# Performance work log

Measured on AMD Instinct MI355X. Metric: run time of the kernel, lower is better.

Reference implementation:

```python
import jax, jax.numpy as jnp
import numpy as np

N_NODES = 50000
N_EDGES = 1600000
DIM = 128
BN_EPS = 1e-5


def setup_inputs() -> dict:
    key = jax.random.key(0)
    k1, k2, k3 = jax.random.split(key, 3)
    x = jax.random.normal(k1, (N_NODES, DIM), dtype=jnp.float32)
    edge_index = jax.random.randint(k2, (2, N_EDGES), 0, N_NODES, dtype=jnp.int32)
    W = jax.random.normal(k3, (DIM, DIM), dtype=jnp.float32) / np.float32(np.sqrt(DIM))
    b = jnp.zeros((DIM,), dtype=jnp.float32)
    gamma = jnp.ones((DIM,), dtype=jnp.float32)
    beta = jnp.zeros((DIM,), dtype=jnp.float32)
    return {"x": x, "W": W, "b": b, "gamma": gamma, "beta": beta, "edge_index": edge_index}


def reference(x, W, b, gamma, beta, edge_index):
    """ResGCNBlock: relu(BN(GCNConv(x, edge_index))) + x (PyG GCNConv semantics)."""
    n = x.shape[0]
    # GCNConv: linear transform first
    h = x @ W  # [N, D]
    # add self-loops
    loop = jnp.arange(n, dtype=edge_index.dtype)
    src = jnp.concatenate([edge_index[0], loop])  # [E+N]
    dst = jnp.concatenate([edge_index[1], loop])
    # symmetric normalization: deg over targets (edge weight = 1)
    deg = jax.ops.segment_sum(jnp.ones_like(dst, dtype=h.dtype), dst, num_segments=n)
    dinv = jax.lax.rsqrt(jnp.maximum(deg, 1e-12))  # deg >= 1 due to self-loops
    norm = dinv[src] * dinv[dst]  # [E+N]
    # gather -> scale -> scatter-add
    agg = jax.ops.segment_sum(h[src] * norm[:, None], dst, num_segments=n) + b  # [N, D]
    # BatchNorm1d (training mode: batch stats over node dim, biased variance)
    mean = jnp.mean(agg, axis=0)
    var = jnp.mean(jnp.square(agg - mean), axis=0)
    y = gamma * (agg - mean) * jax.lax.rsqrt(var + BN_EPS) + beta
    return jax.nn.relu(y) + x
```

## Files before the change

kernel.cpp:

```cpp
#include <hip/hip_runtime.h>

#define DIM 128

__device__ __forceinline__ float bf_to_f(unsigned short v) {
    return __uint_as_float(((unsigned int)v) << 16);
}
__device__ __forceinline__ unsigned short f_to_bf(float f) {
    unsigned int u = __float_as_uint(f);
    u += 0x7FFFu + ((u >> 16) & 1u);
    return (unsigned short)(u >> 16);
}
__device__ __forceinline__ bool probe_bf16(const void* gamma) {
    return *reinterpret_cast<const unsigned int*>(gamma) != 0x3F800000u;
}

__global__ __launch_bounds__(256) void k_deg(const int* __restrict__ ei,
                                             int* __restrict__ deg, int E) {
    int t = blockIdx.x * 256 + threadIdx.x;
    if (t < E) atomicAdd(&deg[ei[E + t]], 1);
}
__global__ __launch_bounds__(256) void k_dinv(const int* __restrict__ deg,
                                              float* __restrict__ dinv, int N) {
    int t = blockIdx.x * 256 + threadIdx.x;
    if (t < N) dinv[t] = rsqrtf((float)deg[t] + 1.0f);
}

#define EPB 4096

__global__ __launch_bounds__(256) void k_cbhist(const int* __restrict__ ei,
                                                int* __restrict__ thist, int E) {
    __shared__ int hist[256];
    const int t = threadIdx.x;
    const int e0 = blockIdx.x * EPB;
    hist[t] = 0;
    __syncthreads();
    #pragma unroll
    for (int u = 0; u < 16; u++) {
        const int i = e0 + t + u * 256;
        if (i < E) atomicAdd(&hist[((unsigned int)ei[E + i]) >> 8], 1);
    }
    __syncthreads();
    if (hist[t] > 0) atomicAdd(&thist[t], hist[t]);
}

__global__ __launch_bounds__(256) void k_bscan2(const int* __restrict__ thist,
                                                int* __restrict__ bbase,
                                                int* __restrict__ ccur) {
    __shared__ int sh[256];
    const int t = threadIdx.x;
    const int v = thist[t];
    sh[t] = v;
    __syncthreads();
    for (int off = 1; off < 256; off <<= 1) {
        int u = (t >= off) ? sh[t - off] : 0;
        __syncthreads();
        sh[t] += u;
        __syncthreads();
    }
    bbase[t + 1] = sh[t];
    ccur[t] = sh[t] - v;
    if (t == 0) bbase[0] = 0;
}

__global__ __launch_bounds__(256) void k_partition(
    const int* __restrict__ ei, int* __restrict__ ccur,
    unsigned int* __restrict__ epart, int E)
{
    __shared__ int hist[256];
    __shared__ int scan_tmp[256];
    __shared__ int lbase[256];
    __shared__ int lcur[256];
    __shared__ int gbase[256];
    __shared__ unsigned int sorted[EPB];
    const int t = threadIdx.x;
    const int e0 = blockIdx.x * EPB;
    const int ecount = min(EPB, E - e0);
    hist[t] = 0; lcur[t] = 0;
    __syncthreads();

    unsigned int ent[16];
    #pragma unroll
    for (int u = 0; u < 16; u++) {
        const int i = e0 + t + u * 256;
        if (i < E) {
            const unsigned int src = (unsigned int)ei[i];
            const unsigned int dst = (unsigned int)ei[E + i];
            const unsigned int cb = dst >> 8;
            ent[u] = src | ((dst & 255u) << 16) | (cb << 24);
            atomicAdd(&hist[cb], 1);
        } else ent[u] = 0xFFFFFFFFu;
    }
    __syncthreads();
    scan_tmp[t] = hist[t];
    __syncthreads();
    for (int off = 1; off < 256; off <<= 1) {
        int v = (t >= off) ? scan_tmp[t - off] : 0;
        __syncthreads();
        scan_tmp[t] += v;
        __syncthreads();
    }
    lbase[t] = scan_tmp[t] - hist[t];
    __syncthreads();
    #pragma unroll
    for (int u = 0; u < 16; u++) {
        if (ent[u] != 0xFFFFFFFFu) {
            const int cb = (int)(ent[u] >> 24);
            const int pos = lbase[cb] + atomicAdd(&lcur[cb], 1);
            sorted[pos] = ent[u];
        }
    }
    if (hist[t] > 0) gbase[t] = atomicAdd(&ccur[t], hist[t]);
    __syncthreads();
    for (int s = t; s < ecount; s += 256) {
        const unsigned int e = sorted[s];
        const int cb = (int)(e >> 24);
        epart[gbase[cb] + (s - lbase[cb])] = e;
    }
}

__global__ __launch_bounds__(256) void k_fine2(
    const unsigned int* __restrict__ epart, const int* __restrict__ bbase,
    int* __restrict__ rowptr, float* __restrict__ dinv,
    int* __restrict__ esrc, int N)
{
    __shared__ int ldeg[256];
    __shared__ int sh[256];
    __shared__ int lex[256];
    __shared__ int lcur[256];
    const int cb = blockIdx.x;
    const int t = threadIdx.x;
    const int beg = bbase[cb];
    const int end = bbase[cb + 1];
    ldeg[t] = 0; lcur[t] = 0;
    __syncthreads();

    for (int i = beg + t; i < end; i += 256)
        atomicAdd(&ldeg[(epart[i] >> 16) & 255u], 1);
    __syncthreads();
    sh[t] = ldeg[t];
    __syncthreads();
    for (int off = 1; off < 256; off <<= 1) {
        int v = (t >= off) ? sh[t - off] : 0;
        __syncthreads();
        sh[t] += v;
        __syncthreads();
    }
    lex[t] = sh[t] - ldeg[t];
    __syncthreads();

    const int node = (cb << 8) + t;
    if (node < N) {
        rowptr[node] = beg + lex[t];
        dinv[node] = rsqrtf((float)ldeg[t] + 1.0f);
        if (node == N - 1) rowptr[N] = beg + lex[t] + ldeg[t];
    }

    for (int i = beg + t; i < end; i += 256) {
        const unsigned int e = epart[i];
        const int d = (int)((e >> 16) & 255u);
        const int pos = beg + lex[d] + atomicAdd(&lcur[d], 1);
        esrc[pos] = (int)(e & 0xFFFFu);
    }
}

__global__ __launch_bounds__(256, 4) void k_gemm(
    const void* __restrict__ xv, const void* __restrict__ Wv,
    const void* __restrict__ bv, const void* __restrict__ probe,
    const float* __restrict__ dinv, unsigned short* __restrict__ h,
    float* __restrict__ agg, int N)
{
    const bool isbf = probe_bf16(probe);
    __shared__ __align__(16) unsigned short Wsb[DIM * 64];
    __shared__ __align__(16) float xs[64 * 132];
    const int t  = threadIdx.x;
    const int ch = blockIdx.x & 1;
    const int r0 = (blockIdx.x >> 1) * 64;

    if (isbf) {
        const unsigned short* W = (const unsigned short*)Wv;
        for (int s = 4 * t; s < DIM * 64; s += 1024) {
            const int k = s >> 6, c = s & 63;
            *reinterpret_cast<ushort4*>(Wsb + s) =
                *reinterpret_cast<const ushort4*>(W + k * DIM + ch * 64 + c);
        }
    } else {
        const float* W = (const float*)Wv;
        for (int s = 4 * t; s < DIM * 64; s += 1024) {
            const int k = s >> 6, c = s & 63;
            const float4 w = *reinterpret_cast<const float4*>(W + k * DIM + ch * 64 + c);
            ushort4 p;
            p.x = f_to_bf(w.x); p.y = f_to_bf(w.y);
            p.z = f_to_bf(w.z); p.w = f_to_bf(w.w);
            *reinterpret_cast<ushort4*>(Wsb + s) = p;
        }
    }
    for (int idx = 4 * t; idx < 64 * DIM; idx += 1024) {
        const int row = idx >> 7, k = idx & 127;
        const int r = r0 + row;
        float4 v = make_float4(0.f, 0.f, 0.f, 0.f);
        if (r < N) {
            if (isbf) {
                ushort4 u = *reinterpret_cast<const ushort4*>(
                    (const unsigned short*)xv + (size_t)r * DIM + k);
                v.x = bf_to_f(u.x); v.y = bf_to_f(u.y);
                v.z = bf_to_f(u.z); v.w = bf_to_f(u.w);
            } else {
                v = *reinterpret_cast<const float4*>((const float*)xv + (size_t)r * DIM + k);
            }
        }
        *reinterpret_cast<float4*>(xs + row * 132 + k) = v;
    }
    __syncthreads();

    const int c4 = t & 15;
    const int rg = t >> 4;
    float acc[4][4] = {{0,0,0,0},{0,0,0,0},{0,0,0,0},{0,0,0,0}};
    #pragma unroll 2
    for (int k = 0; k < DIM; k += 4) {
        const ushort4 wu0 = *reinterpret_cast<const ushort4*>(Wsb + (k + 0) * 64 + 4 * c4);
        const ushort4 wu1 = *reinterpret_cast<const ushort4*>(Wsb + (k + 1) * 64 + 4 * c4);
        const ushort4 wu2 = *reinterpret_cast<const ushort4*>(Wsb + (k + 2) * 64 + 4 * c4);
        const ushort4 wu3 = *reinterpret_cast<const ushort4*>(Wsb + (k + 3) * 64 + 4 * c4);
        float w[4][4];
        w[0][0] = bf_to_f(wu0.x); w[0][1] = bf_to_f(wu0.y);
        w[0][2] = bf_to_f(wu0.z); w[0][3] = bf_to_f(wu0.w);
        w[1][0] = bf_to_f(wu1.x); w[1][1] = bf_to_f(wu1.y);
        w[1][2] = bf_to_f(wu1.z); w[1][3] = bf_to_f(wu1.w);
        w[2][0] = bf_to_f(wu2.x); w[2][1] = bf_to_f(wu2.y);
        w[2][2] = bf_to_f(wu2.z); w[2][3] = bf_to_f(wu2.w);
        w[3][0] = bf_to_f(wu3.x); w[3][1] = bf_to_f(wu3.y);
        w[3][2] = bf_to_f(wu3.z); w[3][3] = bf_to_f(wu3.w);
        #pragma unroll
        for (int j = 0; j < 4; j++) {
            const float4 xk = *reinterpret_cast<const float4*>(&xs[(rg + 16 * j) * 132 + k]);
            #pragma unroll
            for (int cc = 0; cc < 4; cc++) {
                acc[j][cc] = fmaf(xk.x, w[0][cc], acc[j][cc]);
                acc[j][cc] = fmaf(xk.y, w[1][cc], acc[j][cc]);
                acc[j][cc] = fmaf(xk.z, w[2][cc], acc[j][cc]);
                acc[j][cc] = fmaf(xk.w, w[3][cc], acc[j][cc]);
            }
        }
    }
    const int gc = ch * 64 + 4 * c4;
    float4 bc;
    if (isbf) {
        const unsigned short* bb = (const unsigned short*)bv;
        bc.x = bf_to_f(bb[gc]); bc.y = bf_to_f(bb[gc + 1]);
        bc.z = bf_to_f(bb[gc + 2]); bc.w = bf_to_f(bb[gc + 3]);
    } else {
        bc = *reinterpret_cast<const float4*>((const float*)bv + gc);
    }
    #pragma unroll
    for (int j = 0; j < 4; j++) {
        const int r = r0 + rg + 16 * j;
        if (r < N) {
            const float di = dinv[r];
            const float di2 = di * di;
            ushort4 hp;
            hp.x = f_to_bf(acc[j][0]); hp.y = f_to_bf(acc[j][1]);
            hp.z = f_to_bf(acc[j][2]); hp.w = f_to_bf(acc[j][3]);
            *reinterpret_cast<ushort4*>(h + (size_t)r * DIM + gc) = hp;
            float4 av;
            av.x = fmaf(acc[j][0], di2, bc.x);
            av.y = fmaf(acc[j][1], di2, bc.y);
            av.z = fmaf(acc[j][2], di2, bc.z);
            av.w = fmaf(acc[j][3], di2, bc.w);
            *reinterpret_cast<float4*>(agg + (size_t)r * DIM + gc) = av;
        }
    }
}

__device__ __forceinline__ float2 load_h2(const unsigned short* __restrict__ h,
                                          int src, int lane) {
    const unsigned int u = *reinterpret_cast<const unsigned int*>(
        h + (size_t)src * DIM + 2 * lane);
    return make_float2(bf_to_f((unsigned short)(u & 0xFFFFu)),
                       bf_to_f((unsigned short)(u >> 16)));
}

__global__ __launch_bounds__(256) void k_agg(
    const int* __restrict__ rowptr, const int* __restrict__ esrc,
    const unsigned short* __restrict__ h, const float* __restrict__ dinv,
    float* __restrict__ agg, int N)
{
    const int lane = threadIdx.x & 63;
    const int node = (blockIdx.x * 256 + threadIdx.x) >> 6;
    if (node >= N) return;

    const int beg = rowptr[node];
    const int end = rowptr[node + 1];
    const float didst = dinv[node];
    float* arow = agg + (size_t)node * DIM + 2 * lane;
    float2 a = *reinterpret_cast<const float2*>(arow);
    float acc0 = a.x, acc1 = a.y;

    int j = beg;
    for (; j + 8 <= end; j += 8) {
        int s[8];
        #pragma unroll
        for (int u = 0; u < 8; u++) s[u] = esrc[j + u];
        float2 hv[8];
        #pragma unroll
        for (int u = 0; u < 8; u++) hv[u] = load_h2(h, s[u], lane);
        float nn[8];
        #pragma unroll
        for (int u = 0; u < 8; u++) nn[u] = dinv[s[u]] * didst;
        #pragma unroll
        for (int u = 0; u < 8; u++) {
            acc0 = fmaf(hv[u].x, nn[u], acc0);
            acc1 = fmaf(hv[u].y, nn[u], acc1);
        }
    }
    for (; j < end; j++) {
        const int s = esrc[j];
        const float2 h2v = load_h2(h, s, lane);
        const float n = dinv[s] * didst;
        acc0 = fmaf(h2v.x, n, acc0); acc1 = fmaf(h2v.y, n, acc1);
    }
    *reinterpret_cast<float2*>(arow) = make_float2(acc0, acc1);
}

__global__ __launch_bounds__(256) void k_scatter(
    const int* __restrict__ ei, const unsigned short* __restrict__ h,
    const float* __restrict__ dinv, float* __restrict__ agg, int E)
{
    const int w = (blockIdx.x * 256 + threadIdx.x) >> 6;
    if (w >= E) return;
    const int lane = threadIdx.x & 63;
    const int src = ei[w];
    const int dst = ei[E + w];
    const float norm = dinv[src] * dinv[dst];
    const float2 h2 = load_h2(h, src, lane);
    float* a = agg + (size_t)dst * DIM + 2 * lane;
    unsafeAtomicAdd(a + 0, h2.x * norm);
    unsafeAtomicAdd(a + 1, h2.y * norm);
}

__global__ __launch_bounds__(256) void k_stats(
    const float* __restrict__ agg, float* __restrict__ stats, int N, int rpb)
{
    __shared__ float ls[256];
    __shared__ float ls2[256];
    const int c = threadIdx.x & 127;
    const int half = threadIdx.x >> 7;
    const int r0 = blockIdx.x * rpb;
    const int r1 = min(r0 + rpb, N);
    float s = 0.f, s2 = 0.f;
    for (int r = r0 + half; r < r1; r += 2) {
        const float v = agg[(size_t)r * DIM + c];
        s += v;
        s2 = fmaf(v, v, s2);
    }
    ls[threadIdx.x] = s;
    ls2[threadIdx.x] = s2;
    __syncthreads();
    if (threadIdx.x < 128) {
        s  = ls[threadIdx.x]  + ls[threadIdx.x + 128];
        s2 = ls2[threadIdx.x] + ls2[threadIdx.x + 128];
        unsafeAtomicAdd(&stats[c], s);
        unsafeAtomicAdd(&stats[128 + c], s2);
    }
}

__global__ __launch_bounds__(256) void k_out(
    const float* __restrict__ agg, const void* __restrict__ xv,
    const void* __restrict__ gv, const void* __restrict__ bev,
    const float* __restrict__ stats, void* __restrict__ outv,
    float inv_n, int total4)
{
    __shared__ __align__(16) float ssc[128];
    __shared__ __align__(16) float ssh[128];
    const bool isbf = probe_bf16(gv);
    const int tt = threadIdx.x;
    if (tt < 128) {
        const float gamma = isbf ? bf_to_f(((const unsigned short*)gv)[tt])
                                 : ((const float*)gv)[tt];
        const float beta  = isbf ? bf_to_f(((const unsigned short*)bev)[tt])
                                 : ((const float*)bev)[tt];
        const float mean = stats[tt] * inv_n;
        const float var = fmaf(-mean, mean, stats[128 + tt] * inv_n);
        const float rs = rsqrtf(var + 1e-5f);
        const float scale = gamma * rs;
        ssc[tt] = scale;
        ssh[tt] = fmaf(-mean, scale, beta);
    }
    __syncthreads();
    const int t = blockIdx.x * 256 + tt;
    if (t >= total4) return;
    const int c4 = (t & 31) * 4;
    const float4 a = *reinterpret_cast<const float4*>(agg + (size_t)t * 4);
    const float4 sc = *reinterpret_cast<const float4*>(ssc + c4);
    const float4 sh = *reinterpret_cast<const float4*>(ssh + c4);
    float x0, x1, x2, x3;
    if (isbf) {
        const ushort4 u = *reinterpret_cast<const ushort4*>(
            (const unsigned short*)xv + (size_t)t * 4);
        x0 = bf_to_f(u.x); x1 = bf_to_f(u.y); x2 = bf_to_f(u.z); x3 = bf_to_f(u.w);
    } else {
        const float4 xf = *reinterpret_cast<const float4*>((const float*)xv + (size_t)t * 4);
        x0 = xf.x; x1 = xf.y; x2 = xf.z; x3 = xf.w;
    }
    const float y0 = fmaxf(fmaf(a.x, sc.x, sh.x), 0.f) + x0;
    const float y1 = fmaxf(fmaf(a.y, sc.y, sh.y), 0.f) + x1;
    const float y2 = fmaxf(fmaf(a.z, sc.z, sh.z), 0.f) + x2;
    const float y3 = fmaxf(fmaf(a.w, sc.w, sh.w), 0.f) + x3;
    if (isbf) {
        ushort4 o;
        o.x = f_to_bf(y0); o.y = f_to_bf(y1); o.z = f_to_bf(y2); o.w = f_to_bf(y3);
        *reinterpret_cast<ushort4*>((unsigned short*)outv + (size_t)t * 4) = o;
    } else {
        *reinterpret_cast<float4*>((float*)outv + (size_t)t * 4) =
            make_float4(y0, y1, y2, y3);
    }
}

extern "C" void kernel_launch(void* const* d_in, const int* in_sizes, int n_in,
                              void* d_out, int out_size, void* d_ws, size_t ws_size,
                              hipStream_t stream)
{
    const void* x     = d_in[0];
    const void* W     = d_in[1];
    const void* b     = d_in[2];
    const void* gamma = d_in[3];
    const void* beta  = d_in[4];
    const int*  ei    = (const int*)d_in[5];

    const int N = in_sizes[0] / DIM;
    const int E = in_sizes[5] / 2;
    const int nb = (N + 255) >> 8;
    const int nblk = (E + EPB - 1) / EPB;

    char* ws = (char*)d_ws;
    int*          deg    = (int*)(ws + 0);
    float*        stats  = (float*)(ws + 200704);
    int*          thist  = (int*)(ws + 201728);
    float*        dinv   = (float*)(ws + 202752);
    int*          rowptr = (int*)(ws + 403456);
    int*          ccur   = (int*)(ws + 603904);
    int*          bbase  = (int*)(ws + 604928);
    float*        agg    = (float*)(ws + 606976);
    unsigned int* epart  = (unsigned int*)(ws + 606976);
    int*          esrc   = (int*)(ws + 26206976);
    unsigned short* h    = (unsigned short*)d_out;
    const bool use_csr = (ws_size >= 32606976u) && (N <= 65536);

    hipMemsetAsync(ws, 0, 202752, stream);

    if (use_csr) {
        k_cbhist<<<nblk, 256, 0, stream>>>(ei, thist, E);
        k_bscan2<<<1, 256, 0, stream>>>(thist, bbase, ccur);
        k_partition<<<nblk, 256, 0, stream>>>(ei, ccur, epart, E);
        k_fine2<<<nb, 256, 0, stream>>>(epart, bbase, rowptr, dinv, esrc, N);
    } else {
        k_deg<<<(E + 255) / 256, 256, 0, stream>>>(ei, deg, E);
        k_dinv<<<(N + 255) / 256, 256, 0, stream>>>(deg, dinv, N);
    }

    const int nrb = (N + 63) / 64;
    k_gemm<<<nrb * 2, 256, 0, stream>>>(x, W, b, gamma, dinv, h, agg, N);

    if (use_csr) {
        const int nblk_agg = (N * 64 + 255) / 256;
        k_agg<<<nblk_agg, 256, 0, stream>>>(rowptr, esrc, h, dinv, agg, N);
    } else {
        k_scatter<<<(E + 3) / 4, 256, 0, stream>>>(ei, h, dinv, agg, E);
    }

    const int rpb = (N + 255) / 256;
    k_stats<<<256, 256, 0, stream>>>(agg, stats, N, rpb);

    const int total4 = N * DIM / 4;
    k_out<<<(total4 + 255) / 256, 256, 0, stream>>>(
        agg, x, gamma, beta, stats, d_out, 1.0f / (float)N, total4);
}
```

Before: 277.7 us.

## Prescale h by dinv[src] and gather two edges per wave with half-wave split

The GEMM epilogue now stores h already multiplied by dinv of the source row, so the aggregation no longer gathers dinv[src] per edge and just sums bf16 rows, then applies dinv[dst] once. The CSR aggregation kernel splits each 64-lane wave into two halves that gather different edges with 8-byte loads, reads edge indices as int4 vectors, and combines the halves with a cross-lane shuffle at the end. The scatter path is updated to match the prescaled h. The goal is fewer dependent loads and more memory parallelism per edge, in exchange for alignment peeling logic and an extra reduction step. Rounding changes slightly because the normalization is applied before the bf16 conversion.

```diff
diff --git a/kernel.cpp b/kernel.cpp
--- a/kernel.cpp
+++ b/kernel.cpp
@@ -258,8 +258,8 @@
             const float di = dinv[r];
             const float di2 = di * di;
             ushort4 hp;
-            hp.x = f_to_bf(acc[j][0]); hp.y = f_to_bf(acc[j][1]);
-            hp.z = f_to_bf(acc[j][2]); hp.w = f_to_bf(acc[j][3]);
+            hp.x = f_to_bf(acc[j][0] * di); hp.y = f_to_bf(acc[j][1] * di);
+            hp.z = f_to_bf(acc[j][2] * di); hp.w = f_to_bf(acc[j][3] * di);
             *reinterpret_cast<ushort4*>(h + (size_t)r * DIM + gc) = hp;
             float4 av;
             av.x = fmaf(acc[j][0], di2, bc.x);
@@ -285,40 +285,75 @@
     float* __restrict__ agg, int N)
 {
     const int lane = threadIdx.x & 63;
+    const int half = lane >> 5;
+    const int hl   = lane & 31;
     const int node = (blockIdx.x * 256 + threadIdx.x) >> 6;
     if (node >= N) return;
 
     const int beg = rowptr[node];
     const int end = rowptr[node + 1];
     const float didst = dinv[node];
-    float* arow = agg + (size_t)node * DIM + 2 * lane;
-    float2 a = *reinterpret_cast<const float2*>(arow);
-    float acc0 = a.x, acc1 = a.y;
+    float* arow = agg + (size_t)node * DIM + 4 * hl;
+    const float4 seed = *reinterpret_cast<const float4*>(arow);
+
+    float a0 = 0.f, a1 = 0.f, a2 = 0.f, a3 = 0.f;
+
+    auto gather = [&](int src) -> uint2 {
+        return *reinterpret_cast<const uint2*>(h + (size_t)src * DIM + 4 * hl);
+    };
+    auto acc_u2 = [&](uint2 u) {
+        a0 += __uint_as_float(u.x << 16);
+        a1 += __uint_as_float(u.x & 0xFFFF0000u);
+        a2 += __uint_as_float(u.y << 16);
+        a3 += __uint_as_float(u.y & 0xFFFF0000u);
+    };
+    auto do_pair = [&](int s0, int s1) { acc_u2(gather(half ? s1 : s0)); };
+    auto do_one  = [&](int s0) { if (!half) acc_u2(gather(s0)); };
 
     int j = beg;
-    for (; j + 8 <= end; j += 8) {
-        int s[8];
+    if ((j & 1) && j < end) { do_one(esrc[j]); j++; }
+    if ((j & 2) && j + 2 <= end) { do_pair(esrc[j], esrc[j + 1]); j += 2; }
+
+    for (; j + 16 <= end; j += 16) {
+        const int4 A = *reinterpret_cast<const int4*>(esrc + j);
+        const int4 B = *reinterpret_cast<const int4*>(esrc + j + 4);
+        const int4 C = *reinterpret_cast<const int4*>(esrc + j + 8);
+        const int4 D = *reinterpret_cast<const int4*>(esrc + j + 12);
+        int ss[8];
+        ss[0] = half ? A.y : A.x; ss[1] = half ? A.w : A.z;
+        ss[2] = half ? B.y : B.x; ss[3] = half ? B.w : B.z;
+        ss[4] = half ? C.y : C.x; ss[5] = half ? C.w : C.z;
+        ss[6] = half ? D.y : D.x; ss[7] = half ? D.w : D.z;
+        uint2 hv[8];
         #pragma unroll
-        for (int u = 0; u < 8; u++) s[u] = esrc[j + u];
-        float2 hv[8];
+        for (int p = 0; p < 8; p++) hv[p] = gather(ss[p]);
         #pragma unroll
-        for (int u = 0; u < 8; u++) hv[u] = load_h2(h, s[u], lane);
-        float nn[8];
-        #pragma unroll
-        for (int u = 0; u < 8; u++) nn[u] = dinv[s[u]] * didst;
-        #pragma unroll
-        for (int u = 0; u < 8; u++) {
-            acc0 = fmaf(hv[u].x, nn[u], acc0);
-            acc1 = fmaf(hv[u].y, nn[u], acc1);
-        }
-    }
-    for (; j < end; j++) {
-        const int s = esrc[j];
-        const float2 h2v = load_h2(h, s, lane);
-        const float n = dinv[s] * didst;
-        acc0 = fmaf(h2v.x, n, acc0); acc1 = fmaf(h2v.y, n, acc1);
-    }
-    *reinterpret_cast<float2*>(arow) = make_float2(acc0, acc1);
+        for (int p = 0; p < 8; p++) acc_u2(hv[p]);
+    }
+    for (; j + 4 <= end; j += 4) {
+        const int4 A = *reinterpret_cast<const int4*>(esrc + j);
+        const int s0 = half ? A.y : A.x;
+        const int s1 = half ? A.w : A.z;
+        const uint2 h0 = gather(s0);
+        const uint2 h1 = gather(s1);
+        acc_u2(h0); acc_u2(h1);
+    }
+    if (j + 2 <= end) { do_pair(esrc[j], esrc[j + 1]); j += 2; }
+    if (j < end) do_one(esrc[j]);
+
+    a0 += __shfl_xor(a0, 32);
+    a1 += __shfl_xor(a1, 32);
+    a2 += __shfl_xor(a2, 32);
+    a3 += __shfl_xor(a3, 32);
+
+    if (!half) {
+        float4 o;
+        o.x = fmaf(a0, didst, seed.x);
+        o.y = fmaf(a1, didst, seed.y);
+        o.z = fmaf(a2, didst, seed.z);
+        o.w = fmaf(a3, didst, seed.w);
+        *reinterpret_cast<float4*>(arow) = o;
+    }
 }
 
 __global__ __launch_bounds__(256) void k_scatter(
@@ -330,7 +365,7 @@
     const int lane = threadIdx.x & 63;
     const int src = ei[w];
     const int dst = ei[E + w];
-    const float norm = dinv[src] * dinv[dst];
+    const float norm = dinv[dst];
     const float2 h2 = load_h2(h, src, lane);
     float* a = agg + (size_t)dst * DIM + 2 * lane;
     unsafeAtomicAdd(a + 0, h2.x * norm);
```

Result: no change. 273.5 us (-1.5%).

## Fold source normalization into GEMM, restructure CSR aggregation, fuse BN stats

Applied to the files above, without the earlier changes.

The GEMM epilogue now stores h pre-scaled by dinv[src], so the aggregation no longer gathers dinv per edge and only scales by dinv[dst] at the end. The CSR aggregation kernel becomes a grid-stride persistent kernel where each wave handles a node with four 16-lane groups, each loading 16-byte chunks of h rows for different edges, then reduced by shuffles. BatchNorm sum and sum-of-squares are accumulated in the same kernel through LDS and global atomics, which removes the separate stats pass over agg. In exchange it adds a cross-lane reduction per node, atomics on the stats buffer, and bf16 rounding of the pre-scaled h.

```diff
diff --git a/kernel.cpp b/kernel.cpp
--- a/kernel.cpp
+++ b/kernel.cpp
@@ -258,8 +258,8 @@
             const float di = dinv[r];
             const float di2 = di * di;
             ushort4 hp;
-            hp.x = f_to_bf(acc[j][0]); hp.y = f_to_bf(acc[j][1]);
-            hp.z = f_to_bf(acc[j][2]); hp.w = f_to_bf(acc[j][3]);
+            hp.x = f_to_bf(acc[j][0] * di); hp.y = f_to_bf(acc[j][1] * di);
+            hp.z = f_to_bf(acc[j][2] * di); hp.w = f_to_bf(acc[j][3] * di);
             *reinterpret_cast<ushort4*>(h + (size_t)r * DIM + gc) = hp;
             float4 av;
             av.x = fmaf(acc[j][0], di2, bc.x);
@@ -279,46 +279,124 @@
                        bf_to_f((unsigned short)(u >> 16)));
 }
 
-__global__ __launch_bounds__(256) void k_agg(
+__global__ __launch_bounds__(256, 6) void k_agg(
     const int* __restrict__ rowptr, const int* __restrict__ esrc,
     const unsigned short* __restrict__ h, const float* __restrict__ dinv,
-    float* __restrict__ agg, int N)
-{
+    float* __restrict__ agg, float* __restrict__ stats, int N, int nwaves)
+{
+    __shared__ float lst[256];
     const int lane = threadIdx.x & 63;
-    const int node = (blockIdx.x * 256 + threadIdx.x) >> 6;
-    if (node >= N) return;
-
-    const int beg = rowptr[node];
-    const int end = rowptr[node + 1];
-    const float didst = dinv[node];
-    float* arow = agg + (size_t)node * DIM + 2 * lane;
-    float2 a = *reinterpret_cast<const float2*>(arow);
-    float acc0 = a.x, acc1 = a.y;
-
-    int j = beg;
-    for (; j + 8 <= end; j += 8) {
-        int s[8];
-        #pragma unroll
-        for (int u = 0; u < 8; u++) s[u] = esrc[j + u];
-        float2 hv[8];
-        #pragma unroll
-        for (int u = 0; u < 8; u++) hv[u] = load_h2(h, s[u], lane);
-        float nn[8];
-        #pragma unroll
-        for (int u = 0; u < 8; u++) nn[u] = dinv[s[u]] * didst;
-        #pragma unroll
-        for (int u = 0; u < 8; u++) {
-            acc0 = fmaf(hv[u].x, nn[u], acc0);
-            acc1 = fmaf(hv[u].y, nn[u], acc1);
-        }
-    }
-    for (; j < end; j++) {
-        const int s = esrc[j];
-        const float2 h2v = load_h2(h, s, lane);
-        const float n = dinv[s] * didst;
-        acc0 = fmaf(h2v.x, n, acc0); acc1 = fmaf(h2v.y, n, acc1);
-    }
-    *reinterpret_cast<float2*>(arow) = make_float2(acc0, acc1);
+    const int g    = lane >> 4;
+    const int ql   = lane & 15;
+    const int wid  = (blockIdx.x * 256 + threadIdx.x) >> 6;
+
+    lst[threadIdx.x] = 0.f;
+    __syncthreads();
+
+    float ss0 = 0.f, ss1 = 0.f, ss2 = 0.f, ss3 = 0.f;
+    float sq0 = 0.f, sq1 = 0.f, sq2 = 0.f, sq3 = 0.f;
+
+    for (int node = wid; node < N; node += nwaves) {
+        const int beg = rowptr[node];
+        const int end = rowptr[node + 1];
+        const float didst = dinv[node];
+        float a0 = 0.f, a1 = 0.f, a2 = 0.f, a3 = 0.f;
+        float a4 = 0.f, a5 = 0.f, a6 = 0.f, a7 = 0.f;
+
+        auto gath = [&](int s) -> uint4 {
+            return *reinterpret_cast<const uint4*>(h + (size_t)s * DIM + 8 * ql);
+        };
+        auto accum = [&](uint4 u) {
+            a0 += __uint_as_float(u.x << 16);
+            a1 += __uint_as_float(u.x & 0xFFFF0000u);
+            a2 += __uint_as_float(u.y << 16);
+            a3 += __uint_as_float(u.y & 0xFFFF0000u);
+            a4 += __uint_as_float(u.z << 16);
+            a5 += __uint_as_float(u.z & 0xFFFF0000u);
+            a6 += __uint_as_float(u.w << 16);
+            a7 += __uint_as_float(u.w & 0xFFFF0000u);
+        };
+
+        int j = beg;
+        {
+            const int rh = min(end - j, (4 - (j & 3)) & 3);
+            if (rh > 0) {
+                if (g < rh) accum(gath(esrc[j + g]));
+                j += rh;
+            }
+        }
+        for (; j + 32 <= end; j += 32) {
+            const int4 A = *reinterpret_cast<const int4*>(esrc + j + 4 * g);
+            const int4 B = *reinterpret_cast<const int4*>(esrc + j + 16 + 4 * g);
+            const uint4 h0 = gath(A.x);
+            const uint4 h1 = gath(A.y);
+            const uint4 h2 = gath(A.z);
+            const uint4 h3 = gath(A.w);
+            const uint4 h4 = gath(B.x);
+            const uint4 h5 = gath(B.y);
+            const uint4 h6 = gath(B.z);
+            const uint4 h7 = gath(B.w);
+            accum(h0); accum(h1); accum(h2); accum(h3);
+            accum(h4); accum(h5); accum(h6); accum(h7);
+        }
+        if (j + 16 <= end) {
+            const int4 A = *reinterpret_cast<const int4*>(esrc + j + 4 * g);
+            const uint4 h0 = gath(A.x);
+            const uint4 h1 = gath(A.y);
+            const uint4 h2 = gath(A.z);
+            const uint4 h3 = gath(A.w);
+            accum(h0); accum(h1); accum(h2); accum(h3);
+            j += 16;
+        }
+        for (; j + 4 <= end; j += 4) {
+            accum(gath(esrc[j + g]));
+        }
+        {
+            const int rem = end - j;
+            if (g < rem) accum(gath(esrc[j + g]));
+        }
+
+        a0 += __shfl_xor(a0, 16); a0 += __shfl_xor(a0, 32);
+        a1 += __shfl_xor(a1, 16); a1 += __shfl_xor(a1, 32);
+        a2 += __shfl_xor(a2, 16); a2 += __shfl_xor(a2, 32);
+        a3 += __shfl_xor(a3, 16); a3 += __shfl_xor(a3, 32);
+        a4 += __shfl_xor(a4, 16); a4 += __shfl_xor(a4, 32);
+        a5 += __shfl_xor(a5, 16); a5 += __shfl_xor(a5, 32);
+        a6 += __shfl_xor(a6, 16); a6 += __shfl_xor(a6, 32);
+        a7 += __shfl_xor(a7, 16); a7 += __shfl_xor(a7, 32);
+
+        if (g < 2) {
+            float b0, b1, b2, b3;
+            if (g == 0) { b0 = a0; b1 = a1; b2 = a2; b3 = a3; }
+            else        { b0 = a4; b1 = a5; b2 = a6; b3 = a7; }
+            float* arow = agg + (size_t)node * DIM + 8 * ql + 4 * g;
+            const float4 seed = *reinterpret_cast<const float4*>(arow);
+            float4 o;
+            o.x = fmaf(b0, didst, seed.x);
+            o.y = fmaf(b1, didst, seed.y);
+            o.z = fmaf(b2, didst, seed.z);
+            o.w = fmaf(b3, didst, seed.w);
+            *reinterpret_cast<float4*>(arow) = o;
+            ss0 += o.x; sq0 = fmaf(o.x, o.x, sq0);
+            ss1 += o.y; sq1 = fmaf(o.y, o.y, sq1);
+            ss2 += o.z; sq2 = fmaf(o.z, o.z, sq2);
+            ss3 += o.w; sq3 = fmaf(o.w, o.w, sq3);
+        }
+    }
+
+    if (g < 2) {
+        const int c = 8 * ql + 4 * g;
+        atomicAdd(&lst[c + 0], ss0);
+        atomicAdd(&lst[c + 1], ss1);
+        atomicAdd(&lst[c + 2], ss2);
+        atomicAdd(&lst[c + 3], ss3);
+        atomicAdd(&lst[128 + c + 0], sq0);
+        atomicAdd(&lst[128 + c + 1], sq1);
+        atomicAdd(&lst[128 + c + 2], sq2);
+        atomicAdd(&lst[128 + c + 3], sq3);
+    }
+    __syncthreads();
+    unsafeAtomicAdd(&stats[threadIdx.x], lst[threadIdx.x]);
 }
 
 __global__ __launch_bounds__(256) void k_scatter(
@@ -330,7 +408,7 @@
     const int lane = threadIdx.x & 63;
     const int src = ei[w];
     const int dst = ei[E + w];
-    const float norm = dinv[src] * dinv[dst];
+    const float norm = dinv[dst];
     const float2 h2 = load_h2(h, src, lane);
     float* a = agg + (size_t)dst * DIM + 2 * lane;
     unsafeAtomicAdd(a + 0, h2.x * norm);
@@ -461,14 +539,15 @@
     k_gemm<<<nrb * 2, 256, 0, stream>>>(x, W, b, gamma, dinv, h, agg, N);
 
     if (use_csr) {
-        const int nblk_agg = (N * 64 + 255) / 256;
-        k_agg<<<nblk_agg, 256, 0, stream>>>(rowptr, esrc, h, dinv, agg, N);
+        const int nblk_agg = 2048;
+        const int nwaves = nblk_agg * 4;
+        k_agg<<<nblk_agg, 256, 0, stream>>>(rowptr, esrc, h, dinv, agg, stats,
+                                            N, nwaves);
     } else {
         k_scatter<<<(E + 3) / 4, 256, 0, stream>>>(ei, h, dinv, agg, E);
-    }
-
-    const int rpb = (N + 255) / 256;
-    k_stats<<<256, 256, 0, stream>>>(agg, stats, N, rpb);
+        const int rpb = (N + 255) / 256;
+        k_stats<<<256, 256, 0, stream>>>(agg, stats, N, rpb);
+    }
 
     const int total4 = N * DIM / 4;
     k_out<<<(total4 + 255) / 256, 256, 0, stream>>>(
```

Result: slower. 293.7 us (+5.8%).

## Prescale h by dinv in GEMM and simplify CSR aggregation gather

Applied to the files above, without the earlier changes.

Folds the source-side dinv into h during the GEMM epilogue, so the aggregation no longer gathers dinv per edge and applies the destination dinv once at the end. In the CSR path the GEMM skips writing the agg seed; the aggregation starts from the node's own h row and adds the bias in its epilogue. The aggregation loop loads 16 edge indices per wave and broadcasts them with readlane, masking tail edges with a select-multiply, which cuts scalar index loads and a full agg read-modify-write. Rounding h to bf16 after scaling changes numerics slightly, and the padded tail loads redundant rows.

```diff
diff --git a/kernel.cpp b/kernel.cpp
--- a/kernel.cpp
+++ b/kernel.cpp
@@ -167,7 +167,7 @@
     const void* __restrict__ xv, const void* __restrict__ Wv,
     const void* __restrict__ bv, const void* __restrict__ probe,
     const float* __restrict__ dinv, unsigned short* __restrict__ h,
-    float* __restrict__ agg, int N)
+    float* __restrict__ agg, int N, int wr_seed)
 {
     const bool isbf = probe_bf16(probe);
     __shared__ __align__(16) unsigned short Wsb[DIM * 64];
@@ -243,30 +243,32 @@
         }
     }
     const int gc = ch * 64 + 4 * c4;
-    float4 bc;
-    if (isbf) {
-        const unsigned short* bb = (const unsigned short*)bv;
-        bc.x = bf_to_f(bb[gc]); bc.y = bf_to_f(bb[gc + 1]);
-        bc.z = bf_to_f(bb[gc + 2]); bc.w = bf_to_f(bb[gc + 3]);
-    } else {
-        bc = *reinterpret_cast<const float4*>((const float*)bv + gc);
-    }
     #pragma unroll
     for (int j = 0; j < 4; j++) {
         const int r = r0 + rg + 16 * j;
         if (r < N) {
             const float di = dinv[r];
-            const float di2 = di * di;
             ushort4 hp;
-            hp.x = f_to_bf(acc[j][0]); hp.y = f_to_bf(acc[j][1]);
-            hp.z = f_to_bf(acc[j][2]); hp.w = f_to_bf(acc[j][3]);
+            hp.x = f_to_bf(acc[j][0] * di); hp.y = f_to_bf(acc[j][1] * di);
+            hp.z = f_to_bf(acc[j][2] * di); hp.w = f_to_bf(acc[j][3] * di);
             *reinterpret_cast<ushort4*>(h + (size_t)r * DIM + gc) = hp;
-            float4 av;
-            av.x = fmaf(acc[j][0], di2, bc.x);
-            av.y = fmaf(acc[j][1], di2, bc.y);
-            av.z = fmaf(acc[j][2], di2, bc.z);
-            av.w = fmaf(acc[j][3], di2, bc.w);
-            *reinterpret_cast<float4*>(agg + (size_t)r * DIM + gc) = av;
+            if (wr_seed) {
+                float4 bc;
+                if (isbf) {
+                    const unsigned short* bb = (const unsigned short*)bv;
+                    bc.x = bf_to_f(bb[gc]); bc.y = bf_to_f(bb[gc + 1]);
+                    bc.z = bf_to_f(bb[gc + 2]); bc.w = bf_to_f(bb[gc + 3]);
+                } else {
+                    bc = *reinterpret_cast<const float4*>((const float*)bv + gc);
+                }
+                const float di2 = di * di;
+                float4 av;
+                av.x = fmaf(acc[j][0], di2, bc.x);
+                av.y = fmaf(acc[j][1], di2, bc.y);
+                av.z = fmaf(acc[j][2], di2, bc.z);
+                av.w = fmaf(acc[j][3], di2, bc.w);
+                *reinterpret_cast<float4*>(agg + (size_t)r * DIM + gc) = av;
+            }
         }
     }
 }
@@ -282,43 +284,59 @@
 __global__ __launch_bounds__(256) void k_agg(
     const int* __restrict__ rowptr, const int* __restrict__ esrc,
     const unsigned short* __restrict__ h, const float* __restrict__ dinv,
+    const void* __restrict__ bv, const void* __restrict__ probe,
     float* __restrict__ agg, int N)
 {
     const int lane = threadIdx.x & 63;
-    const int node = (blockIdx.x * 256 + threadIdx.x) >> 6;
+    const int node = __builtin_amdgcn_readfirstlane(
+        (int)((blockIdx.x * 256 + threadIdx.x) >> 6));
     if (node >= N) return;
 
     const int beg = rowptr[node];
     const int end = rowptr[node + 1];
     const float didst = dinv[node];
-    float* arow = agg + (size_t)node * DIM + 2 * lane;
-    float2 a = *reinterpret_cast<const float2*>(arow);
-    float acc0 = a.x, acc1 = a.y;
-
-    int j = beg;
-    for (; j + 8 <= end; j += 8) {
-        int s[8];
+    const unsigned int* __restrict__ hu = (const unsigned int*)h;
+
+    float a0 = 0.f, a1 = 0.f;
+
+    {
+        const unsigned int v = hu[(size_t)node * 64 + lane];
+        a0 += __uint_as_float(v << 16);
+        a1 += __uint_as_float(v & 0xFFFF0000u);
+    }
+
+    const int lm = end - 1;
+    for (int j = beg; j < end; j += 16) {
+        const int myidx = esrc[min(j + (lane & 15), lm)];
+        unsigned int uv[16];
         #pragma unroll
-        for (int u = 0; u < 8; u++) s[u] = esrc[j + u];
-        float2 hv[8];
+        for (int u = 0; u < 16; u++) {
+            const int s = __builtin_amdgcn_readlane(myidx, u);
+            uv[u] = hu[(size_t)s * 64 + lane];
+        }
         #pragma unroll
-        for (int u = 0; u < 8; u++) hv[u] = load_h2(h, s[u], lane);
-        float nn[8];
-        #pragma unroll
-        for (int u = 0; u < 8; u++) nn[u] = dinv[s[u]] * didst;
-        #pragma unroll
-        for (int u = 0; u < 8; u++) {
-            acc0 = fmaf(hv[u].x, nn[u], acc0);
-            acc1 = fmaf(hv[u].y, nn[u], acc1);
-        }
-    }
-    for (; j < end; j++) {
-        const int s = esrc[j];
-        const float2 h2v = load_h2(h, s, lane);
-        const float n = dinv[s] * didst;
-        acc0 = fmaf(h2v.x, n, acc0); acc1 = fmaf(h2v.y, n, acc1);
-    }
-    *reinterpret_cast<float2*>(arow) = make_float2(acc0, acc1);
+        for (int u = 0; u < 16; u++) {
+            const float sel = (j + u < end) ? 1.0f : 0.0f;
+            a0 = fmaf(__uint_as_float(uv[u] << 16), sel, a0);
+            a1 = fmaf(__uint_as_float(uv[u] & 0xFFFF0000u), sel, a1);
+        }
+    }
+
+    const int gc = 2 * lane;
+    float b0, b1;
+    if (probe_bf16(probe)) {
+        const unsigned int bb = *reinterpret_cast<const unsigned int*>(
+            (const unsigned short*)bv + gc);
+        b0 = bf_to_f((unsigned short)(bb & 0xFFFFu));
+        b1 = bf_to_f((unsigned short)(bb >> 16));
+    } else {
+        const float2 bf = *reinterpret_cast<const float2*>((const float*)bv + gc);
+        b0 = bf.x; b1 = bf.y;
+    }
+    float2 o;
+    o.x = fmaf(a0, didst, b0);
+    o.y = fmaf(a1, didst, b1);
+    *reinterpret_cast<float2*>(agg + (size_t)node * DIM + gc) = o;
 }
 
 __global__ __launch_bounds__(256) void k_scatter(
@@ -330,7 +348,7 @@
     const int lane = threadIdx.x & 63;
     const int src = ei[w];
     const int dst = ei[E + w];
-    const float norm = dinv[src] * dinv[dst];
+    const float norm = dinv[dst];
     const float2 h2 = load_h2(h, src, lane);
     float* a = agg + (size_t)dst * DIM + 2 * lane;
     unsafeAtomicAdd(a + 0, h2.x * norm);
@@ -458,11 +476,13 @@
     }
 
     const int nrb = (N + 63) / 64;
-    k_gemm<<<nrb * 2, 256, 0, stream>>>(x, W, b, gamma, dinv, h, agg, N);
+    k_gemm<<<nrb * 2, 256, 0, stream>>>(x, W, b, gamma, dinv, h, agg, N,
+                                        use_csr ? 0 : 1);
 
     if (use_csr) {
         const int nblk_agg = (N * 64 + 255) / 256;
-        k_agg<<<nblk_agg, 256, 0, stream>>>(rowptr, esrc, h, dinv, agg, N);
+        k_agg<<<nblk_agg, 256, 0, stream>>>(rowptr, esrc, h, dinv, b, gamma,
+                                            agg, N);
     } else {
         k_scatter<<<(E + 3) / 4, 256, 0, stream>>>(ei, h, dinv, agg, E);
     }
```

Result: faster. 264.9 us (-4.6%).
